# Optimization experiments

Hardware: AMD Instinct MI355X
Metric: run time of the kernel (lower is better)

The kernel has to match this reference:

```python
import jax, jax.numpy as jnp
import numpy as np

N, D_TOK, K = 8192, 256, 16


def knn_idx(xyz, k):
    # squared pairwise distances, diagonal excluded (loop=False)
    sq = jnp.sum(xyz * xyz, axis=-1)                      # [N]
    dist = sq[:, None] - 2.0 * (xyz @ xyz.T) + sq[None, :]  # [N,N]
    dist = dist + jnp.eye(xyz.shape[0], dtype=xyz.dtype) * jnp.asarray(1e10, xyz.dtype)
    _, idx = jax.lax.top_k(-dist, k)                      # [N,k] nearest neighbors j for each target i
    return idx


def edgeconv(x, nbr, W1, b1, W2, b2):
    # EdgeConv message: nn(concat(x_i, x_j - x_i)), aggr = max over neighbors
    n, d = x.shape
    k = nbr.shape[1]
    xi = x[:, None, :]                                    # [N,1,D]
    xj = x[nbr]                                           # [N,k,D] gather
    msg = jnp.concatenate([jnp.broadcast_to(xi, (n, k, d)), xj - xi], axis=-1)  # [N,k,2D]
    h = jax.nn.relu(msg @ W1 + b1) @ W2 + b2              # [N,k,token_dim]
    return jnp.max(h, axis=1)                             # [N,token_dim]


def setup_inputs() -> dict:
    key = jax.random.key(0)
    ks = jax.random.split(key, 10)
    d_in = 2 * (D_TOK + 3)
    s1 = 1.0 / np.sqrt(d_in)
    s2 = 1.0 / np.sqrt(D_TOK)
    return {
        "xyz": jax.random.normal(ks[0], (N, 3), dtype=jnp.float32),
        "feat": jax.random.normal(ks[1], (N, D_TOK), dtype=jnp.float32),
        "W1a": jax.random.normal(ks[2], (d_in, D_TOK), dtype=jnp.float32) * s1,
        "b1a": jnp.zeros((D_TOK,), dtype=jnp.float32),
        "W2a": jax.random.normal(ks[3], (D_TOK, D_TOK), dtype=jnp.float32) * s2,
        "b2a": jnp.zeros((D_TOK,), dtype=jnp.float32),
        "W1b": jax.random.normal(ks[4], (d_in, D_TOK), dtype=jnp.float32) * s1,
        "b1b": jnp.zeros((D_TOK,), dtype=jnp.float32),
        "W2b": jax.random.normal(ks[5], (D_TOK, D_TOK), dtype=jnp.float32) * s2,
        "b2b": jnp.zeros((D_TOK,), dtype=jnp.float32),
    }


def reference(xyz, feat, W1a, b1a, W2a, b2a, W1b, b1b, W2b, b2b):
    nbr = knn_idx(xyz, K)                                 # [N,k], built once, reused by both convs
    x = jnp.concatenate([feat, xyz], axis=-1)             # [N, D_TOK+3]
    x = edgeconv(x, nbr, W1a, b1a, W2a, b2a)              # [N, D_TOK]
    x = jnp.concatenate([x, xyz], axis=-1)                # [N, D_TOK+3]
    x = edgeconv(x, nbr, W1b, b1b, W2b, b2b)              # [N, D_TOK]
    return x
```

## Files before the change

### kernel.cpp

```cpp
#include <hip/hip_runtime.h>
#include <cfloat>

#define N_PTS 8192
#define DTOK 256
#define KNN 16

typedef __attribute__((ext_vector_type(8))) short short8;
typedef __attribute__((ext_vector_type(4))) float float4v;
typedef __attribute__((ext_vector_type(2))) float float2v;

__device__ inline short f2bf(float f) {
  unsigned u = __float_as_uint(f);
  u += 0x7fffu + ((u >> 16) & 1u);
  return (short)(u >> 16);
}
__device__ inline float bf2f(short h) {
  return __uint_as_float(((unsigned)(unsigned short)h) << 16);
}

__device__ inline float2v pk_mul(float2v a, float2v b) {
  float2v d;
  asm("v_pk_mul_f32 %0, %1, %2" : "=v"(d) : "v"(a), "v"(b));
  return d;
}
__device__ inline float2v pk_fma(float2v a, float2v b, float2v c) {
  float2v d;
  asm("v_pk_fma_f32 %0, %1, %2, %3" : "=v"(d) : "v"(a), "v"(b), "v"(c));
  return d;
}
__device__ inline float2v pk_add(float2v a, float2v b) {
  float2v d;
  asm("v_pk_add_f32 %0, %1, %2" : "=v"(d) : "v"(a), "v"(b));
  return d;
}
__device__ inline float2v pk_sub(float2v a, float2v b) {
  float2v d;
  asm("v_pk_add_f32 %0, %1, %2 neg_lo:[0,1] neg_hi:[0,1]"
      : "=v"(d) : "v"(a), "v"(b));
  return d;
}

__global__ __launch_bounds__(256) void knn_prep_kernel(
    const float* __restrict__ xyz, float4* __restrict__ xyz4) {
  const int i = blockIdx.x * 256 + threadIdx.x;
  float x = xyz[3 * i], y = xyz[3 * i + 1], z = xyz[3 * i + 2];
  float sq = __fadd_rn(__fadd_rn(__fmul_rn(x, x), __fmul_rn(y, y)),
                       __fmul_rn(z, z));
  xyz4[i] = make_float4(x, y, z, sq);
}

__device__ inline void insert_group(float d, int base, float t, int lane,
                                    float& sd, int& sj, float& s15) {
  unsigned long long m = __ballot(d <= t);
  while (m) {
    const int src = __ffsll(m) - 1;
    m &= m - 1;
    const float dc = __shfl(d, src);
    if (dc < s15) {
      const int jc = base + src;
      const unsigned long long bm = __ballot(sd <= dc) & 0xFFFFull;
      const int pos = (int)__popcll(bm);
      const float pu = __shfl_up(sd, 1);
      const int ju = __shfl_up(sj, 1);
      if (lane < 16) {
        if (lane > pos)        { sd = pu; sj = ju; }
        else if (lane == pos)  { sd = dc; sj = jc; }
      }
      s15 = __shfl(sd, 15);
    }
  }
}

#define KCH 512
#define NCH (N_PTS / KCH)

__global__ __launch_bounds__(256) void knn_select_kernel(
    const float4* __restrict__ xyz4, int* __restrict__ nbr) {
  __shared__ float4 sA[2][4][64];
  __shared__ float4 sB[2][4][64];
  const int tid = threadIdx.x;
  const int lane = tid & 63;
  const int wave = tid >> 6;
  const int i0 = blockIdx.x * 8 + wave * 2;
  const int i1 = i0 + 1;

  const float4 q0 = xyz4[i0];
  const float4 q1 = xyz4[i1];
  const float2v x02 = {q0.x, q0.x}, y02 = {q0.y, q0.y};
  const float2v z02 = {q0.z, q0.z}, s02 = {q0.w, q0.w};
  const float2v x12 = {q1.x, q1.x}, y12 = {q1.y, q1.y};
  const float2v z12 = {q1.z, q1.z}, s12 = {q1.w, q1.w};
  const float2v two2 = {2.0f, 2.0f};

  const int ib128 = i0 & ~127;
  const int ih0 = (i0 >> 6) & 1, il0 = i0 & 63;
  const int ih1 = (i1 >> 6) & 1, il1 = i1 & 63;

  const int sgj = wave * 128 + lane;

  {
    const float4 c0 = xyz4[sgj];
    const float4 c1 = xyz4[sgj + 64];
    sA[0][wave][lane] = make_float4(c0.x, c1.x, c0.y, c1.y);
    sB[0][wave][lane] = make_float4(c0.z, c1.z, c0.w, c1.w);
  }
  __syncthreads();

  float a00 = FLT_MAX, a01 = FLT_MAX, a10 = FLT_MAX, a11 = FLT_MAX;
  for (int c = 0; c < NCH; ++c) {
    const int b = c & 1;
    float4 n0, n1;
    if (c < NCH - 1) {
      n0 = xyz4[(c + 1) * KCH + sgj];
      n1 = xyz4[(c + 1) * KCH + sgj + 64];
    }
    const int cbase = c * KCH;
    #pragma unroll
    for (int ps = 0; ps < 4; ++ps) {
      const float4 a = sA[b][ps][lane];
      const float4 bb = sB[b][ps][lane];
      const float2v px = {a.x, a.y}, py = {a.z, a.w};
      const float2v pz = {bb.x, bb.y}, pw = {bb.z, bb.w};
      const float2v dot0 = pk_fma(z02, pz, pk_fma(y02, py, pk_mul(x02, px)));
      float2v d0 = pk_add(pk_sub(s02, pk_mul(two2, dot0)), pw);
      const float2v dot1 = pk_fma(z12, pz, pk_fma(y12, py, pk_mul(x12, px)));
      float2v d1 = pk_add(pk_sub(s12, pk_mul(two2, dot1)), pw);
      if (cbase + ps * 128 == ib128) {
        if (lane == il0) {
          if (ih0) d0.y = __fadd_rn(d0.y, 1e10f);
          else     d0.x = __fadd_rn(d0.x, 1e10f);
        }
        if (lane == il1) {
          if (ih1) d1.y = __fadd_rn(d1.y, 1e10f);
          else     d1.x = __fadd_rn(d1.x, 1e10f);
        }
      }
      a00 = fminf(a00, d0.x);
      a01 = fminf(a01, d0.y);
      a10 = fminf(a10, d1.x);
      a11 = fminf(a11, d1.y);
    }
    if (c < NCH - 1) {
      sA[b ^ 1][wave][lane] = make_float4(n0.x, n1.x, n0.y, n1.y);
      sB[b ^ 1][wave][lane] = make_float4(n0.z, n1.z, n0.w, n1.w);
    }
    __syncthreads();
  }

  float v0 = fminf(a00, a01);
  float v1 = fminf(a10, a11);
  #pragma unroll
  for (int k = 2; k <= 64; k <<= 1) {
    #pragma unroll
    for (int j = k >> 1; j > 0; j >>= 1) {
      const float o0 = __shfl_xor(v0, j, 64);
      const float o1 = __shfl_xor(v1, j, 64);
      const bool keepmin = ((lane & k) == 0) == ((lane & j) == 0);
      v0 = keepmin ? fminf(v0, o0) : fmaxf(v0, o0);
      v1 = keepmin ? fminf(v1, o1) : fmaxf(v1, o1);
    }
  }
  const float t0 = __shfl(v0, 15, 64);
  const float t1 = __shfl(v1, 15, 64);

  float sd0 = FLT_MAX, sd1 = FLT_MAX;
  int sj0 = 0, sj1 = 0;
  float s150 = FLT_MAX, s151 = FLT_MAX;

  {
    const float4 c0 = xyz4[sgj];
    const float4 c1 = xyz4[sgj + 64];
    sA[0][wave][lane] = make_float4(c0.x, c1.x, c0.y, c1.y);
    sB[0][wave][lane] = make_float4(c0.z, c1.z, c0.w, c1.w);
  }
  __syncthreads();

  for (int c = 0; c < NCH; ++c) {
    const int b = c & 1;
    float4 n0, n1;
    if (c < NCH - 1) {
      n0 = xyz4[(c + 1) * KCH + sgj];
      n1 = xyz4[(c + 1) * KCH + sgj + 64];
    }
    const int cbase = c * KCH;

    float2v dd0[4], dd1[4];
    #pragma unroll
    for (int ps = 0; ps < 4; ++ps) {
      const float4 a = sA[b][ps][lane];
      const float4 bb = sB[b][ps][lane];
      const float2v px = {a.x, a.y}, py = {a.z, a.w};
      const float2v pz = {bb.x, bb.y}, pw = {bb.z, bb.w};
      const float2v dot0 = pk_fma(z02, pz, pk_fma(y02, py, pk_mul(x02, px)));
      dd0[ps] = pk_add(pk_sub(s02, pk_mul(two2, dot0)), pw);
      const float2v dot1 = pk_fma(z12, pz, pk_fma(y12, py, pk_mul(x12, px)));
      dd1[ps] = pk_add(pk_sub(s12, pk_mul(two2, dot1)), pw);
      if (cbase + ps * 128 == ib128) {
        if (lane == il0) {
          if (ih0) dd0[ps].y = __fadd_rn(dd0[ps].y, 1e10f);
          else     dd0[ps].x = __fadd_rn(dd0[ps].x, 1e10f);
        }
        if (lane == il1) {
          if (ih1) dd1[ps].y = __fadd_rn(dd1[ps].y, 1e10f);
          else     dd1[ps].x = __fadd_rn(dd1[ps].x, 1e10f);
        }
      }
    }

    #pragma unroll
    for (int ps = 0; ps < 4; ++ps) {
      const int base = cbase + ps * 128;
      insert_group(dd0[ps].x, base,      t0, lane, sd0, sj0, s150);
      insert_group(dd0[ps].y, base + 64, t0, lane, sd0, sj0, s150);
      insert_group(dd1[ps].x, base,      t1, lane, sd1, sj1, s151);
      insert_group(dd1[ps].y, base + 64, t1, lane, sd1, sj1, s151);
    }

    if (c < NCH - 1) {
      sA[b ^ 1][wave][lane] = make_float4(n0.x, n1.x, n0.y, n1.y);
      sB[b ^ 1][wave][lane] = make_float4(n0.z, n1.z, n0.w, n1.w);
    }
    __syncthreads();
  }
  if (lane < 16) {
    nbr[i0 * KNN + lane] = sj0;
    nbr[i1 * KNN + lane] = sj1;
  }
}

__global__ __launch_bounds__(256) void convert_w_kernel(
    const float* __restrict__ W1, short* __restrict__ bhi,
    short* __restrict__ blo) {
  const int n = blockIdx.x;
  const int k = threadIdx.x;
  const float v = (n < 256) ? W1[k * DTOK + n]
                            : W1[(259 + k) * DTOK + (n - 256)];
  short h = f2bf(v);
  bhi[n * 256 + k] = h;
  blo[n * 256 + k] = f2bf(v - bf2f(h));
}

__global__ __launch_bounds__(256, 2) void pq_gemm_fused_kernel(
    const float* __restrict__ A, const short* __restrict__ Bthi,
    const short* __restrict__ Btlo, const float* __restrict__ xyz,
    const float* __restrict__ W1, const float* __restrict__ b1,
    float* __restrict__ R, float* __restrict__ Q) {
  __shared__ short Ahi[64][32], Alo[64][32];
  __shared__ short Bhi[128][32], Blo[128][32];
  __shared__ float Qs[64][65];
  __shared__ float sx[64][3];
  __shared__ float swz[6][64];
  __shared__ float sb1[64];

  const int tid = threadIdx.x;
  const int lane = tid & 63;
  const int wave = tid >> 6;
  const int l15 = lane & 15;
  const int quad = lane >> 4;
  const int mh = wave & 1;
  const int qh = wave >> 1;
  const int m0 = blockIdx.x * 64;
  const int np0 = blockIdx.y * 64;

  if (tid < 64) {
    sx[tid][0] = xyz[(m0 + tid) * 3];
    sx[tid][1] = xyz[(m0 + tid) * 3 + 1];
    sx[tid][2] = xyz[(m0 + tid) * 3 + 2];
  } else if (tid < 128) {
    int n = tid - 64;
    sb1[n] = b1[np0 + n];
    #pragma unroll
    for (int r = 0; r < 3; ++r) {
      swz[r][n] = W1[(256 + r) * DTOK + np0 + n];
      swz[3 + r][n] = W1[(515 + r) * DTOK + np0 + n];
    }
  }

  float4v acc[2][4];
  #pragma unroll
  for (int mf = 0; mf < 2; ++mf)
    #pragma unroll
    for (int nf = 0; nf < 4; ++nf)
      #pragma unroll
      for (int e = 0; e < 4; ++e) acc[mf][nf][e] = 0.f;

  const int ar = tid >> 2;
  const int ak = (tid & 3) * 8;

  #pragma unroll 1
  for (int kc = 0; kc < 8; ++kc) {
    const int k0 = kc * 32;
    __syncthreads();
    {
      const float* asrc = A + (size_t)(m0 + ar) * 256 + k0 + ak;
      float4 a0 = *(const float4*)asrc;
      float4 a1 = *(const float4*)(asrc + 4);
      float v[8] = {a0.x, a0.y, a0.z, a0.w, a1.x, a1.y, a1.z, a1.w};
      short8 h8, l8;
      #pragma unroll
      for (int e = 0; e < 8; ++e) {
        short h = f2bf(v[e]);
        h8[e] = h;
        l8[e] = f2bf(v[e] - bf2f(h));
      }
      *(short8*)(&Ahi[ar][ak]) = h8;
      *(short8*)(&Alo[ar][ak]) = l8;
    }
    #pragma unroll
    for (int l = 0; l < 4; ++l) {
      const int rem = tid + 256 * (l & 1);
      const int row = rem >> 2;
      const int koff = (rem & 3) * 8;
      const int n = (row < 64) ? (np0 + row) : (256 + np0 + row - 64);
      const short* src = ((l < 2) ? Bthi : Btlo) + (size_t)n * 256 + k0 + koff;
      short8 vv = *(const short8*)src;
      if (l < 2) *(short8*)(&Bhi[row][koff]) = vv;
      else       *(short8*)(&Blo[row][koff]) = vv;
    }
    __syncthreads();

    short8 ah[2], al[2], bh[4], bl[4];
    #pragma unroll
    for (int mf = 0; mf < 2; ++mf) {
      ah[mf] = *(const short8*)(&Ahi[mh * 32 + mf * 16 + l15][quad * 8]);
      al[mf] = *(const short8*)(&Alo[mh * 32 + mf * 16 + l15][quad * 8]);
    }
    #pragma unroll
    for (int nf = 0; nf < 4; ++nf) {
      bh[nf] = *(const short8*)(&Bhi[qh * 64 + nf * 16 + l15][quad * 8]);
      bl[nf] = *(const short8*)(&Blo[qh * 64 + nf * 16 + l15][quad * 8]);
    }
    #pragma unroll
    for (int mf = 0; mf < 2; ++mf)
      #pragma unroll
      for (int nf = 0; nf < 4; ++nf) {
        acc[mf][nf] = __builtin_amdgcn_mfma_f32_16x16x32_bf16(
            ah[mf], bh[nf], acc[mf][nf], 0, 0, 0);
        acc[mf][nf] = __builtin_amdgcn_mfma_f32_16x16x32_bf16(
            ah[mf], bl[nf], acc[mf][nf], 0, 0, 0);
        acc[mf][nf] = __builtin_amdgcn_mfma_f32_16x16x32_bf16(
            al[mf], bh[nf], acc[mf][nf], 0, 0, 0);
      }
  }

  if (qh == 1) {
    #pragma unroll
    for (int mf = 0; mf < 2; ++mf)
      #pragma unroll
      for (int nf = 0; nf < 4; ++nf)
        #pragma unroll
        for (int e = 0; e < 4; ++e) {
          int row = mh * 32 + mf * 16 + quad * 4 + e;
          int col = nf * 16 + l15;
          float q = acc[mf][nf][e] + sx[row][0] * swz[3][col] +
                    sx[row][1] * swz[4][col] + sx[row][2] * swz[5][col];
          Qs[row][col] = q;
          Q[(size_t)(m0 + row) * DTOK + np0 + col] = q;
        }
  }
  __syncthreads();
  if (qh == 0) {
    #pragma unroll
    for (int mf = 0; mf < 2; ++mf)
      #pragma unroll
      for (int nf = 0; nf < 4; ++nf)
        #pragma unroll
        for (int e = 0; e < 4; ++e) {
          int row = mh * 32 + mf * 16 + quad * 4 + e;
          int col = nf * 16 + l15;
          float p = acc[mf][nf][e] + sx[row][0] * swz[0][col] +
                    sx[row][1] * swz[1][col] + sx[row][2] * swz[2][col];
          R[(size_t)(m0 + row) * DTOK + np0 + col] =
              (p + sb1[col]) - Qs[row][col];
        }
  }
}

#define EP 8

__global__ __launch_bounds__(256, 2) void edge_mfma_kernel(
    const float* __restrict__ R, const float* __restrict__ Q,
    const int* __restrict__ nbr, const float* __restrict__ W2,
    const float* __restrict__ b2, float* __restrict__ out,
    int num_groups, int groups_per_block) {
  __shared__ short Hs[EP * KNN * DTOK];
  const int lane = threadIdx.x & 63;
  const int wave = threadIdx.x >> 6;
  const int l15 = lane & 15;
  const int quad = lane >> 4;

  short8 bfr[4][8];
  #pragma unroll
  for (int nt_i = 0; nt_i < 4; ++nt_i) {
    const int n = (wave * 4 + nt_i) * 16 + l15;
    #pragma unroll
    for (int kt = 0; kt < 8; ++kt) {
      short8 f;
      #pragma unroll
      for (int jj = 0; jj < 8; ++jj) {
        int k = kt * 32 + quad * 8 + jj;
        f[jj] = f2bf(W2[k * DTOK + n]);
      }
      bfr[nt_i][kt] = f;
    }
  }

  const int wc8 = lane >> 1;
  const int wsub = (lane & 1) * 4;

  for (int gi = 0; gi < groups_per_block; ++gi) {
    const int g = blockIdx.x + gi * gridDim.x;
    if (g >= num_groups) break;
    const int i0 = g * EP;

    {
      const int ia = i0 + wave * 2;
      const int jr0 = nbr[ia * KNN + l15];
      const int jr1 = nbr[(ia + 1) * KNN + l15];
      const float4 ri0 = ((const float4*)(R + (size_t)ia * DTOK))[lane];
      const float4 ri1 = ((const float4*)(R + (size_t)(ia + 1) * DTOK))[lane];
      #pragma unroll
      for (int pp = 0; pp < 2; ++pp) {
        const float4 ri = pp ? ri1 : ri0;
        const int jr = pp ? jr1 : jr0;
        #pragma unroll
        for (int k = 0; k < KNN; ++k) {
          const int j = __shfl(jr, k, 16);
          const float4 qj = ((const float4*)(Q + (size_t)j * DTOK))[lane];
          const int r = wave * 32 + pp * 16 + k;
          uint2 pk;
          pk.x = ((unsigned)(unsigned short)f2bf(fmaxf(ri.x + qj.x, 0.f))) |
                 (((unsigned)(unsigned short)f2bf(fmaxf(ri.y + qj.y, 0.f))) << 16);
          pk.y = ((unsigned)(unsigned short)f2bf(fmaxf(ri.z + qj.z, 0.f))) |
                 (((unsigned)(unsigned short)f2bf(fmaxf(ri.w + qj.w, 0.f))) << 16);
          *(uint2*)(&Hs[r * DTOK + ((wc8 ^ (r & 7)) << 3) + wsub]) = pk;
        }
      }
    }
    __syncthreads();

    #pragma unroll
    for (int mp = 0; mp < 4; ++mp) {
      float4v acc[2][4];
      #pragma unroll
      for (int mi = 0; mi < 2; ++mi)
        #pragma unroll
        for (int nt_i = 0; nt_i < 4; ++nt_i)
          #pragma unroll
          for (int e = 0; e < 4; ++e) acc[mi][nt_i][e] = 0.f;

      #pragma unroll
      for (int kt = 0; kt < 8; ++kt) {
        const int pc = ((kt * 4 + quad) ^ (l15 & 7)) << 3;
        const short8 a0 = *(const short8*)(
            &Hs[((mp * 2 + 0) * 16 + l15) * DTOK + pc]);
        const short8 a1 = *(const short8*)(
            &Hs[((mp * 2 + 1) * 16 + l15) * DTOK + pc]);
        #pragma unroll
        for (int nt_i = 0; nt_i < 4; ++nt_i) {
          acc[0][nt_i] = __builtin_amdgcn_mfma_f32_16x16x32_bf16(
              a0, bfr[nt_i][kt], acc[0][nt_i], 0, 0, 0);
          acc[1][nt_i] = __builtin_amdgcn_mfma_f32_16x16x32_bf16(
              a1, bfr[nt_i][kt], acc[1][nt_i], 0, 0, 0);
        }
      }

      #pragma unroll
      for (int mi = 0; mi < 2; ++mi) {
        #pragma unroll
        for (int nt_i = 0; nt_i < 4; ++nt_i) {
          float rm = fmaxf(fmaxf(acc[mi][nt_i][0], acc[mi][nt_i][1]),
                           fmaxf(acc[mi][nt_i][2], acc[mi][nt_i][3]));
          rm = fmaxf(rm, __shfl_xor(rm, 16, 64));
          rm = fmaxf(rm, __shfl_xor(rm, 32, 64));
          if (lane < 16) {
            const int i = i0 + mp * 2 + mi;
            const int n = (wave * 4 + nt_i) * 16 + lane;
            out[(size_t)i * DTOK + n] = rm + b2[n];
          }
        }
      }
    }
    __syncthreads();
  }
}

extern "C" void kernel_launch(void* const* d_in, const int* in_sizes, int n_in,
                              void* d_out, int out_size, void* d_ws,
                              size_t ws_size, hipStream_t stream) {
  const float* xyz = (const float*)d_in[0];
  const float* feat = (const float*)d_in[1];
  const float* W1a = (const float*)d_in[2];
  const float* b1a = (const float*)d_in[3];
  const float* W2a = (const float*)d_in[4];
  const float* b2a = (const float*)d_in[5];
  const float* W1b = (const float*)d_in[6];
  const float* b1b = (const float*)d_in[7];
  const float* W2b = (const float*)d_in[8];
  const float* b2b = (const float*)d_in[9];
  float* out = (float*)d_out;

  char* w = (char*)d_ws;
  const size_t SZ_NBR = (size_t)N_PTS * KNN * sizeof(int);
  const size_t MB = 1024 * 1024;
  int* nbr = (int*)w;
  char* w1 = w + SZ_NBR;
  float4* xyz4 = (float4*)w1;
  float* R = (float*)(w1 + 8 * MB);
  float* Q = (float*)(w + SZ_NBR + 16 * MB);
  short* Bthi = (short*)(w + SZ_NBR + 24 * MB);
  short* Btlo = Bthi + 512 * 256;
  float* bufC = out;

  knn_prep_kernel<<<N_PTS / 256, 256, 0, stream>>>(xyz, xyz4);
  knn_select_kernel<<<N_PTS / 8, 256, 0, stream>>>(xyz4, nbr);

  const int num_groups = N_PTS / EP;
  const int nblocks = 512;

  convert_w_kernel<<<512, 256, 0, stream>>>(W1a, Bthi, Btlo);
  pq_gemm_fused_kernel<<<dim3(N_PTS / 64, 4), 256, 0, stream>>>(
      feat, Bthi, Btlo, xyz, W1a, b1a, R, Q);
  edge_mfma_kernel<<<nblocks, 256, 0, stream>>>(R, Q, nbr, W2a, b2a, bufC,
                                                num_groups, 2);

  convert_w_kernel<<<512, 256, 0, stream>>>(W1b, Bthi, Btlo);
  pq_gemm_fused_kernel<<<dim3(N_PTS / 64, 4), 256, 0, stream>>>(
      bufC, Bthi, Btlo, xyz, W1b, b1b, R, Q);
  edge_mfma_kernel<<<nblocks, 256, 0, stream>>>(R, Q, nbr, W2b, b2b, out,
                                                num_groups, 2);
}
```

Baseline: 236.8 us.

## Drop LDS staging and barriers from KNN insertion pass; fuse distance subtract into FMA

The second (insertion) pass of the KNN select kernel no longer stages candidate points through double-buffered shared memory with block barriers. Each wave now streams 64 points per iteration straight from global memory, prefetching the next group into registers, and computes scalar distances. The first pass replaces the separate packed mul and sub with a single packed FMA by -2. This removes per-chunk __syncthreads and LDS traffic in the divergent insertion loop, so waves no longer wait on each other. In exchange, every wave re-reads xyz4 from global/L2 and the insertion-pass distance math becomes scalar instead of packed.

```diff
diff --git a/kernel.cpp b/kernel.cpp
--- a/kernel.cpp
+++ b/kernel.cpp
@@ -31,12 +31,6 @@
 __device__ inline float2v pk_add(float2v a, float2v b) {
   float2v d;
   asm("v_pk_add_f32 %0, %1, %2" : "=v"(d) : "v"(a), "v"(b));
-  return d;
-}
-__device__ inline float2v pk_sub(float2v a, float2v b) {
-  float2v d;
-  asm("v_pk_add_f32 %0, %1, %2 neg_lo:[0,1] neg_hi:[0,1]"
-      : "=v"(d) : "v"(a), "v"(b));
   return d;
 }
 
@@ -90,7 +84,7 @@
   const float2v z02 = {q0.z, q0.z}, s02 = {q0.w, q0.w};
   const float2v x12 = {q1.x, q1.x}, y12 = {q1.y, q1.y};
   const float2v z12 = {q1.z, q1.z}, s12 = {q1.w, q1.w};
-  const float2v two2 = {2.0f, 2.0f};
+  const float2v n2 = {-2.0f, -2.0f};
 
   const int ib128 = i0 & ~127;
   const int ih0 = (i0 >> 6) & 1, il0 = i0 & 63;
@@ -109,10 +103,10 @@
   float a00 = FLT_MAX, a01 = FLT_MAX, a10 = FLT_MAX, a11 = FLT_MAX;
   for (int c = 0; c < NCH; ++c) {
     const int b = c & 1;
-    float4 n0, n1;
+    float4 nx0, nx1;
     if (c < NCH - 1) {
-      n0 = xyz4[(c + 1) * KCH + sgj];
-      n1 = xyz4[(c + 1) * KCH + sgj + 64];
+      nx0 = xyz4[(c + 1) * KCH + sgj];
+      nx1 = xyz4[(c + 1) * KCH + sgj + 64];
     }
     const int cbase = c * KCH;
     #pragma unroll
@@ -121,11 +115,14 @@
       const float4 bb = sB[b][ps][lane];
       const float2v px = {a.x, a.y}, py = {a.z, a.w};
       const float2v pz = {bb.x, bb.y}, pw = {bb.z, bb.w};
-      const float2v dot0 = pk_fma(z02, pz, pk_fma(y02, py, pk_mul(x02, px)));
-      float2v d0 = pk_add(pk_sub(s02, pk_mul(two2, dot0)), pw);
-      const float2v dot1 = pk_fma(z12, pz, pk_fma(y12, py, pk_mul(x12, px)));
-      float2v d1 = pk_add(pk_sub(s12, pk_mul(two2, dot1)), pw);
-      if (cbase + ps * 128 == ib128) {
+      const bool selfg = (cbase + ps * 128 == ib128);
+      const float2v dot0 =
+          pk_fma(z02, pz, pk_fma(y02, py, pk_mul(x02, px)));
+      float2v d0 = pk_add(pk_fma(n2, dot0, s02), pw);
+      const float2v dot1 =
+          pk_fma(z12, pz, pk_fma(y12, py, pk_mul(x12, px)));
+      float2v d1 = pk_add(pk_fma(n2, dot1, s12), pw);
+      if (selfg) {
         if (lane == il0) {
           if (ih0) d0.y = __fadd_rn(d0.y, 1e10f);
           else     d0.x = __fadd_rn(d0.x, 1e10f);
@@ -141,8 +138,8 @@
       a11 = fminf(a11, d1.y);
     }
     if (c < NCH - 1) {
-      sA[b ^ 1][wave][lane] = make_float4(n0.x, n1.x, n0.y, n1.y);
-      sB[b ^ 1][wave][lane] = make_float4(n0.z, n1.z, n0.w, n1.w);
+      sA[b ^ 1][wave][lane] = make_float4(nx0.x, nx1.x, nx0.y, nx1.y);
+      sB[b ^ 1][wave][lane] = make_float4(nx0.z, nx1.z, nx0.w, nx1.w);
     }
     __syncthreads();
   }
@@ -167,61 +164,30 @@
   int sj0 = 0, sj1 = 0;
   float s150 = FLT_MAX, s151 = FLT_MAX;
 
-  {
-    const float4 c0 = xyz4[sgj];
-    const float4 c1 = xyz4[sgj + 64];
-    sA[0][wave][lane] = make_float4(c0.x, c1.x, c0.y, c1.y);
-    sB[0][wave][lane] = make_float4(c0.z, c1.z, c0.w, c1.w);
-  }
-  __syncthreads();
-
-  for (int c = 0; c < NCH; ++c) {
-    const int b = c & 1;
-    float4 n0, n1;
-    if (c < NCH - 1) {
-      n0 = xyz4[(c + 1) * KCH + sgj];
-      n1 = xyz4[(c + 1) * KCH + sgj + 64];
-    }
-    const int cbase = c * KCH;
-
-    float2v dd0[4], dd1[4];
-    #pragma unroll
-    for (int ps = 0; ps < 4; ++ps) {
-      const float4 a = sA[b][ps][lane];
-      const float4 bb = sB[b][ps][lane];
-      const float2v px = {a.x, a.y}, py = {a.z, a.w};
-      const float2v pz = {bb.x, bb.y}, pw = {bb.z, bb.w};
-      const float2v dot0 = pk_fma(z02, pz, pk_fma(y02, py, pk_mul(x02, px)));
-      dd0[ps] = pk_add(pk_sub(s02, pk_mul(two2, dot0)), pw);
-      const float2v dot1 = pk_fma(z12, pz, pk_fma(y12, py, pk_mul(x12, px)));
-      dd1[ps] = pk_add(pk_sub(s12, pk_mul(two2, dot1)), pw);
-      if (cbase + ps * 128 == ib128) {
-        if (lane == il0) {
-          if (ih0) dd0[ps].y = __fadd_rn(dd0[ps].y, 1e10f);
-          else     dd0[ps].x = __fadd_rn(dd0[ps].x, 1e10f);
-        }
-        if (lane == il1) {
-          if (ih1) dd1[ps].y = __fadd_rn(dd1[ps].y, 1e10f);
-          else     dd1[ps].x = __fadd_rn(dd1[ps].x, 1e10f);
-        }
-      }
-    }
-
-    #pragma unroll
-    for (int ps = 0; ps < 4; ++ps) {
-      const int base = cbase + ps * 128;
-      insert_group(dd0[ps].x, base,      t0, lane, sd0, sj0, s150);
-      insert_group(dd0[ps].y, base + 64, t0, lane, sd0, sj0, s150);
-      insert_group(dd1[ps].x, base,      t1, lane, sd1, sj1, s151);
-      insert_group(dd1[ps].y, base + 64, t1, lane, sd1, sj1, s151);
-    }
-
-    if (c < NCH - 1) {
-      sA[b ^ 1][wave][lane] = make_float4(n0.x, n1.x, n0.y, n1.y);
-      sB[b ^ 1][wave][lane] = make_float4(n0.z, n1.z, n0.w, n1.w);
-    }
-    __syncthreads();
-  }
+  const int gself = i0 >> 6;
+
+  float4 pc = xyz4[lane];
+  #pragma unroll 2
+  for (int grp = 0; grp < N_PTS / 64; ++grp) {
+    float4 pn;
+    if (grp < N_PTS / 64 - 1) pn = xyz4[(grp + 1) * 64 + lane];
+
+    const float dot0 = fmaf(q0.z, pc.z, fmaf(q0.y, pc.y,
+                                             __fmul_rn(q0.x, pc.x)));
+    float d0 = __fadd_rn(__fmaf_rn(-2.0f, dot0, q0.w), pc.w);
+    const float dot1 = fmaf(q1.z, pc.z, fmaf(q1.y, pc.y,
+                                             __fmul_rn(q1.x, pc.x)));
+    float d1 = __fadd_rn(__fmaf_rn(-2.0f, dot1, q1.w), pc.w);
+    if (grp == gself) {
+      if (lane == il0) d0 = __fadd_rn(d0, 1e10f);
+      if (lane == il1) d1 = __fadd_rn(d1, 1e10f);
+    }
+
+    insert_group(d0, grp * 64, t0, lane, sd0, sj0, s150);
+    insert_group(d1, grp * 64, t1, lane, sd1, sj1, s151);
+    pc = pn;
+  }
+
   if (lane < 16) {
     nbr[i0 * KNN + lane] = sj0;
     nbr[i1 * KNN + lane] = sj1;
```

Result: faster. 229.7 us (-3.0%).
